# Kernel tuning notes

Hardware: AMD Instinct MI355X
Metric: run time of the kernel (lower is better)

Reference implementation:

```python
import jax, jax.numpy as jnp
import numpy as np

B, S, D, H = 2, 2048, 1024, 16
ND = D // H  # head dim = 64


def setup_inputs() -> dict:
    key = jax.random.key(0)
    ks = jax.random.split(key, 11)
    scale = 1.0 / np.sqrt(D)
    inp = {
        "q": jax.random.normal(ks[0], (B, S, D), dtype=jnp.float32),
        "k": jax.random.normal(ks[1], (B, S, D), dtype=jnp.float32),
        "v": jax.random.normal(ks[2], (B, S, D), dtype=jnp.float32),
        # causal mask, broadcast over batch and heads
        "mask": jnp.tril(jnp.ones((S, S), dtype=jnp.int32))[None, None, :, :],
        "Wq": jax.random.normal(ks[3], (D, D), dtype=jnp.float32) * scale,
        "bq": jnp.zeros((D,), dtype=jnp.float32),
        "Wk": jax.random.normal(ks[4], (D, D), dtype=jnp.float32) * scale,
        "bk": jnp.zeros((D,), dtype=jnp.float32),
        "Wv": jax.random.normal(ks[5], (D, D), dtype=jnp.float32) * scale,
        "bv": jnp.zeros((D,), dtype=jnp.float32),
        "Wo": jax.random.normal(ks[6], (D, D), dtype=jnp.float32) * scale,
        "bo": jnp.zeros((D,), dtype=jnp.float32),
    }
    return inp


def reference(q, k, v, mask, Wq, bq, Wk, bk, Wv, bv, Wo, bo):
    batch, seq_len, _ = q.shape
    # torch nn.Linear: x @ W.T + b
    qh = (q @ Wq.T + bq).reshape(batch, seq_len, H, ND).transpose(0, 2, 1, 3)
    kh = (k @ Wk.T + bk).reshape(batch, seq_len, H, ND).transpose(0, 2, 1, 3)
    vh = (v @ Wv.T + bv).reshape(batch, seq_len, H, ND).transpose(0, 2, 1, 3)
    # [B,H,S,S] scores
    score = jnp.einsum("bhqd,bhkd->bhqk", qh, kh) / jnp.sqrt(jnp.float32(ND))
    score = jnp.where(mask == 0, jnp.float32(-1e9), score)
    score = jax.nn.softmax(score, axis=-1)
    out = jnp.einsum("bhqk,bhkd->bhqd", score, vh)
    out = out.transpose(0, 2, 1, 3).reshape(batch, seq_len, D)
    return out @ Wo.T + bo
```

## Files before the change

### kernel.cpp

```cpp
#include <hip/hip_runtime.h>
#include <hip/hip_bf16.h>
#include <stdint.h>

#define S_LEN 2048
#define DMODEL 1024
#define NHEAD 16
#define HDIM 64
#define BATCH 2

typedef __bf16 bf16_t;
typedef __attribute__((ext_vector_type(8))) __bf16 bf16x8;
typedef __attribute__((ext_vector_type(4))) __bf16 bf16x4;
typedef __attribute__((ext_vector_type(4))) float f32x4;
typedef __attribute__((ext_vector_type(16))) float f32x16;
typedef __attribute__((ext_vector_type(4))) uint32_t u32x4;

#define LOG2E 1.44269504088896340736f

__device__ __forceinline__ void gload_lds16(const void* g, void* l) {
  __builtin_amdgcn_global_load_lds(
      (const __attribute__((address_space(1))) uint32_t*)g,
      (__attribute__((address_space(3))) uint32_t*)l, 16, 0, 0);
}

__global__ __launch_bounds__(256) void convert_all(
    const float* __restrict__ q, const float* __restrict__ k, const float* __restrict__ v,
    const float* __restrict__ wq, const float* __restrict__ wk, const float* __restrict__ wv,
    const float* __restrict__ wo,
    bf16_t* __restrict__ qb, bf16_t* __restrict__ kb, bf16_t* __restrict__ vb,
    bf16_t* __restrict__ wqb, bf16_t* __restrict__ wkb, bf16_t* __restrict__ wvb,
    bf16_t* __restrict__ wob)
{
  const size_t M1 = 1048576;
  size_t e = ((size_t)blockIdx.x * 256 + threadIdx.x) * 4;
  const float* src; bf16_t* dst; size_t off;
  if      (e <  4*M1) { src = q;  dst = qb;  off = e;         }
  else if (e <  8*M1) { src = k;  dst = kb;  off = e - 4*M1;  }
  else if (e < 12*M1) { src = v;  dst = vb;  off = e - 8*M1;  }
  else if (e < 13*M1) { src = wq; dst = wqb; off = e - 12*M1; }
  else if (e < 14*M1) { src = wk; dst = wkb; off = e - 13*M1; }
  else if (e < 15*M1) { src = wv; dst = wvb; off = e - 14*M1; }
  else                { src = wo; dst = wob; off = e - 15*M1; }
  float4 f = *reinterpret_cast<const float4*>(src + off);
  bf16x4 o;
  o[0] = (bf16_t)f.x; o[1] = (bf16_t)f.y; o[2] = (bf16_t)f.z; o[3] = (bf16_t)f.w;
  *reinterpret_cast<bf16x4*>(dst + off) = o;
}

__device__ __forceinline__ void gemm_body(
    const bf16_t* __restrict__ A, const bf16_t* __restrict__ W,
    const float* __restrict__ bias, bf16_t* __restrict__ outb,
    float* __restrict__ outf, int M, int N, int K, float scale, int packmode)
{
  __shared__ bf16_t As[128 * 32];
  __shared__ bf16_t Bs[128 * 32];
  int tid = threadIdx.x;
  int w = tid >> 6, lane = tid & 63;
  int lr = lane & 15, lg = lane >> 4;
  int wr = w >> 1, wc = w & 1;
  int m0 = blockIdx.x * 128, n0 = blockIdx.y * 128;

  f32x4 acc[4][4];
#pragma unroll
  for (int a = 0; a < 4; ++a)
#pragma unroll
    for (int bq = 0; bq < 4; ++bq) acc[a][bq] = (f32x4){0.f, 0.f, 0.f, 0.f};

  int col_st = (lane & 3) * 8;

  for (int kt = 0; kt < K; kt += 32) {
#pragma unroll
    for (int it = 0; it < 2; ++it) {
      int chunkbase = (w * 2 + it) * 512;
      int row = (w * 2 + it) * 16 + (lane >> 2);
      gload_lds16(A + (size_t)(m0 + row) * K + kt + col_st, &As[chunkbase]);
      gload_lds16(W + (size_t)(n0 + row) * K + kt + col_st, &Bs[chunkbase]);
    }
    __syncthreads();
    bf16x8 af[4], bfv[4];
#pragma unroll
    for (int mf = 0; mf < 4; ++mf)
      af[mf] = *reinterpret_cast<const bf16x8*>(&As[(wr * 64 + mf * 16 + lr) * 32 + lg * 8]);
#pragma unroll
    for (int nf = 0; nf < 4; ++nf)
      bfv[nf] = *reinterpret_cast<const bf16x8*>(&Bs[(wc * 64 + nf * 16 + lr) * 32 + lg * 8]);
#pragma unroll
    for (int mf = 0; mf < 4; ++mf)
#pragma unroll
      for (int nf = 0; nf < 4; ++nf)
        acc[mf][nf] = __builtin_amdgcn_mfma_f32_16x16x32_bf16(af[mf], bfv[nf], acc[mf][nf], 0, 0, 0);
    __syncthreads();
  }

#pragma unroll
  for (int mf = 0; mf < 4; ++mf) {
#pragma unroll
    for (int nf = 0; nf < 4; ++nf) {
      int col = n0 + wc * 64 + nf * 16 + lr;
      float bcol = bias[col];
#pragma unroll
      for (int i = 0; i < 4; ++i) {
        int row = m0 + wr * 64 + mf * 16 + lg * 4 + i;
        float vv = (acc[mf][nf][i] + bcol) * scale;
        if (outf) {
          outf[(size_t)row * N + col] = vv;
        } else if (packmode == 0) {
          outb[(size_t)row * N + col] = (bf16_t)vv;
        } else if (packmode == 1) {
          int hh = col >> 6, dh = col & 63;
          int ks = dh >> 4, hi2 = (dh >> 3) & 1, jj = dh & 7;
          int bb2 = row >> 11, sK = row & 2047;
          int bh = bb2 * 16 + hh;
          size_t off = ((size_t)(bh * 64 + (sK >> 5)) * 8 + ks * 2 + hi2) * 256
                     + (size_t)(sK & 31) * 8 + jj;
          outb[off] = (bf16_t)vv;
        } else {
          int hh = col >> 6, d = col & 63;
          int db = d >> 5, dlo = d & 31;
          int bb2 = row >> 11, sK = row & 2047;
          int t32 = sK >> 5, kvin = sK & 31;
          int s2 = kvin >> 4, hi2 = (kvin >> 3) & 1, jj = kvin & 7;
          int bh = bb2 * 16 + hh;
          size_t off = ((size_t)(bh * 64 + t32) * 4 + s2 * 2 + db) * 512
                     + (size_t)(hi2 * 32 + dlo) * 8 + jj;
          outb[off] = (bf16_t)vv;
        }
      }
    }
  }
}

__global__ __launch_bounds__(256) void gemm_proj(
    const bf16_t* __restrict__ qb, const bf16_t* __restrict__ kb, const bf16_t* __restrict__ vb,
    const bf16_t* __restrict__ wqb, const bf16_t* __restrict__ wkb, const bf16_t* __restrict__ wvb,
    const float* __restrict__ bq, const float* __restrict__ bk, const float* __restrict__ bv,
    bf16_t* __restrict__ Qp, bf16_t* __restrict__ Kpk, bf16_t* __restrict__ Vpk)
{
  int z = blockIdx.z;
  const bf16_t* A = (z == 0) ? qb : (z == 1) ? kb : vb;
  const bf16_t* W = (z == 0) ? wqb : (z == 1) ? wkb : wvb;
  const float* bias = (z == 0) ? bq : (z == 1) ? bk : bv;
  bf16_t* o = (z == 0) ? Qp : (z == 1) ? Kpk : Vpk;
  float scale = (z == 0) ? 0.125f * LOG2E : 1.0f;
  gemm_body(A, W, bias, o, nullptr, BATCH * S_LEN, DMODEL, DMODEL, scale, z);
}

__global__ __launch_bounds__(256) void gemm_out(
    const bf16_t* __restrict__ O, const bf16_t* __restrict__ wob,
    const float* __restrict__ bo, float* __restrict__ out)
{
  gemm_body(O, wob, bo, nullptr, out, BATCH * S_LEN, DMODEL, DMODEL, 1.0f, 0);
}

__global__ __launch_bounds__(256, 2) void attn_fwd(
    const bf16_t* __restrict__ Qp, const bf16_t* __restrict__ Kpk,
    const bf16_t* __restrict__ Vpk, bf16_t* __restrict__ O)
{
  int flat = blockIdx.x;
  int bh = flat & 31, qp = flat >> 5;
  int b = bh >> 4, h = bh & 15;
  int tid = threadIdx.x, wv = tid >> 6, lane = tid & 63;
  int ql = lane & 31, hi = lane >> 5;
  int s = wv >> 1, hf = wv & 1;

  __shared__ float Om[2][64][35];

  const bf16_t* Kbh = Kpk + (size_t)bh * 131072 + lane * 8;
  const bf16_t* Vbh = Vpk + (size_t)bh * 131072 + lane * 8;

  for (int p = 0; p < 2; ++p) {
    int qt64 = p ? (31 - qp) : qp;
    int qbase = qt64 * 64 + s * 32;
    int q_row = qbase + ql;
    int t_diag = qbase >> 5;
    int t0 = hf ? (qt64 + 1) : 0;
    int t1 = hf ? (2 * qt64 + 2) : (qt64 + 1);
    t1 = (t1 < t_diag + 1) ? t1 : (t_diag + 1);

    const bf16_t* Qb = Qp + ((size_t)b * S_LEN + q_row) * DMODEL + h * HDIM + hi * 8;
    bf16x8 qf[4];
#pragma unroll
    for (int ks = 0; ks < 4; ++ks)
      qf[ks] = *reinterpret_cast<const bf16x8*>(Qb + ks * 16);

    f32x16 oacc0 = (f32x16)(0.0f);
    f32x16 oacc1 = (f32x16)(0.0f);
    float m = -1e30f, l = 0.f;

    for (int t = t0; t < t1; ++t) {
      const bf16_t* Kt = Kbh + (size_t)t * 2048;
      const bf16_t* Vt = Vbh + (size_t)t * 2048;

      bf16x8 kf[4], vf[4];
#pragma unroll
      for (int f = 0; f < 4; ++f)
        kf[f] = *reinterpret_cast<const bf16x8*>(Kt + f * 512);
#pragma unroll
      for (int f = 0; f < 4; ++f)
        vf[f] = *reinterpret_cast<const bf16x8*>(Vt + f * 512);

      f32x16 sa = (f32x16)(0.0f);
      __builtin_amdgcn_s_setprio(1);
      sa = __builtin_amdgcn_mfma_f32_32x32x16_bf16(kf[0], qf[0], sa, 0, 0, 0);
      sa = __builtin_amdgcn_mfma_f32_32x32x16_bf16(kf[1], qf[1], sa, 0, 0, 0);
      sa = __builtin_amdgcn_mfma_f32_32x32x16_bf16(kf[2], qf[2], sa, 0, 0, 0);
      sa = __builtin_amdgcn_mfma_f32_32x32x16_bf16(kf[3], qf[3], sa, 0, 0, 0);
      __builtin_amdgcn_s_setprio(0);

      if (t == t_diag) {
#pragma unroll
        for (int r = 0; r < 16; ++r) {
          int kvl = (r & 3) + 8 * (r >> 2) + 4 * hi;
          if (kvl > ql) sa[r] = -1e30f;
        }
      }

      float lmax = sa[0];
#pragma unroll
      for (int r = 1; r < 16; ++r) lmax = fmaxf(lmax, sa[r]);
      if (__any(lmax > m + 8.f)) {
        float mx = fmaxf(lmax, __shfl_xor(lmax, 32));
        float mn = fmaxf(m, mx);
        float rsc = __builtin_amdgcn_exp2f(m - mn);
        m = mn; l *= rsc;
        oacc0 *= rsc;
        oacc1 *= rsc;
      }

      float pr[16];
      float psum = 0.f;
#pragma unroll
      for (int r = 0; r < 16; ++r) {
        pr[r] = __builtin_amdgcn_exp2f(sa[r] - m);
        psum += pr[r];
      }
      l += psum;

      uint32_t w[8];
#pragma unroll
      for (int kk = 0; kk < 8; ++kk) {
        bf16_t plo = (bf16_t)pr[2 * kk], phi = (bf16_t)pr[2 * kk + 1];
        w[kk] = (uint32_t)__builtin_bit_cast(unsigned short, plo)
              | ((uint32_t)__builtin_bit_cast(unsigned short, phi) << 16);
      }

      __builtin_amdgcn_s_setprio(1);
      {
        uint32_t u0  = hi ? w[2] : w[0], u1  = hi ? w[3] : w[1];
        uint32_t sd0 = hi ? w[0] : w[2], sd1 = hi ? w[1] : w[3];
        uint32_t x0 = __shfl_xor(sd0, 32), x1 = __shfl_xor(sd1, 32);
        u32x4 pw = { hi ? x0 : u0, hi ? x1 : u1, hi ? u0 : x0, hi ? u1 : x1 };
        bf16x8 pf = __builtin_bit_cast(bf16x8, pw);
        oacc0 = __builtin_amdgcn_mfma_f32_32x32x16_bf16(vf[0], pf, oacc0, 0, 0, 0);
        oacc1 = __builtin_amdgcn_mfma_f32_32x32x16_bf16(vf[1], pf, oacc1, 0, 0, 0);
      }
      {
        uint32_t u0  = hi ? w[6] : w[4], u1  = hi ? w[7] : w[5];
        uint32_t sd0 = hi ? w[4] : w[6], sd1 = hi ? w[5] : w[7];
        uint32_t x0 = __shfl_xor(sd0, 32), x1 = __shfl_xor(sd1, 32);
        u32x4 pw = { hi ? x0 : u0, hi ? x1 : u1, hi ? u0 : x0, hi ? u1 : x1 };
        bf16x8 pf = __builtin_bit_cast(bf16x8, pw);
        oacc0 = __builtin_amdgcn_mfma_f32_32x32x16_bf16(vf[2], pf, oacc0, 0, 0, 0);
        oacc1 = __builtin_amdgcn_mfma_f32_32x32x16_bf16(vf[3], pf, oacc1, 0, 0, 0);
      }
      __builtin_amdgcn_s_setprio(0);
    }

    if (hf) {
      Om[s][lane][0] = m;
      Om[s][lane][1] = l;
#pragma unroll
      for (int r = 0; r < 16; ++r) {
        Om[s][lane][2 + r]  = oacc0[r];
        Om[s][lane][18 + r] = oacc1[r];
      }
    }
    __syncthreads();
    if (!hf) {
      float mB = Om[s][lane][0], lB = Om[s][lane][1];
      float mAB = fmaxf(m, mB);
      float fA = __builtin_amdgcn_exp2f(m - mAB);
      float fB = __builtin_amdgcn_exp2f(mB - mAB);
      l = l * fA + lB * fB;
#pragma unroll
      for (int r = 0; r < 16; ++r) {
        oacc0[r] = oacc0[r] * fA + Om[s][lane][2 + r]  * fB;
        oacc1[r] = oacc1[r] * fA + Om[s][lane][18 + r] * fB;
      }
      l += __shfl_xor(l, 32);
      float inv = 1.0f / l;
      bf16_t* ob = O + ((size_t)b * S_LEN + q_row) * DMODEL + h * HDIM;
#pragma unroll
      for (int g = 0; g < 4; ++g) {
        bf16x4 ov0, ov1;
#pragma unroll
        for (int i = 0; i < 4; ++i) {
          ov0[i] = (bf16_t)(oacc0[4 * g + i] * inv);
          ov1[i] = (bf16_t)(oacc1[4 * g + i] * inv);
        }
        *reinterpret_cast<bf16x4*>(ob + 8 * g + 4 * hi)      = ov0;
        *reinterpret_cast<bf16x4*>(ob + 32 + 8 * g + 4 * hi) = ov1;
      }
    }
    __syncthreads();
  }
}

extern "C" void kernel_launch(void* const* d_in, const int* in_sizes, int n_in,
                              void* d_out, int out_size, void* d_ws, size_t ws_size,
                              hipStream_t stream) {
  const float* q  = (const float*)d_in[0];
  const float* k  = (const float*)d_in[1];
  const float* v  = (const float*)d_in[2];
  const float* Wq = (const float*)d_in[4];
  const float* bq = (const float*)d_in[5];
  const float* Wk = (const float*)d_in[6];
  const float* bk = (const float*)d_in[7];
  const float* Wv = (const float*)d_in[8];
  const float* bv = (const float*)d_in[9];
  const float* Wo = (const float*)d_in[10];
  const float* bo = (const float*)d_in[11];
  float* out = (float*)d_out;

  const size_t MB = 1u << 20;
  char* base = (char*)d_ws;
  bf16_t* qb  = (bf16_t*)(base + 0 * MB);
  bf16_t* kb  = (bf16_t*)(base + 8 * MB);
  bf16_t* vb  = (bf16_t*)(base + 16 * MB);
  bf16_t* wqb = (bf16_t*)(base + 24 * MB);
  bf16_t* wkb = (bf16_t*)(base + 26 * MB);
  bf16_t* wvb = (bf16_t*)(base + 28 * MB);
  bf16_t* wob = (bf16_t*)(base + 30 * MB);
  bf16_t* Qp  = (bf16_t*)(base + 32 * MB);
  bf16_t* Kpk = (bf16_t*)(base + 40 * MB);
  bf16_t* Vpk = (bf16_t*)(base + 48 * MB);
  bf16_t* Ob  = (bf16_t*)(base + 56 * MB);

  convert_all<<<16384, 256, 0, stream>>>(q, k, v, Wq, Wk, Wv, Wo,
                                         qb, kb, vb, wqb, wkb, wvb, wob);
  gemm_proj<<<dim3(32, 8, 3), 256, 0, stream>>>(qb, kb, vb, wqb, wkb, wvb,
                                                bq, bk, bv, Qp, Kpk, Vpk);
  attn_fwd<<<512, 256, 0, stream>>>(Qp, Kpk, Vpk, Ob);
  gemm_out<<<dim3(32, 8), 256, 0, stream>>>(Ob, wob, bo, out);
}
```

Before: 113.2 us.

## Rewrite QKV projection GEMM with 256x256 tiles, double-buffered swizzled LDS

The QKV projection GEMM now uses 512-thread blocks with 256x256 output tiles and K-step 64. Global-to-LDS loads are double-buffered and issued in halves between compute phases, with explicit vmcnt waits and barriers. LDS reads use an XOR swizzle to avoid bank conflicts, and the MFMA bursts run at raised priority. The goal is to hide load latency and raise data reuse per tile. The cost is a grid of only 192 blocks, which may underfill the GPU, plus 128KB of LDS per block.

```diff
diff --git a/kernel.cpp b/kernel.cpp
--- a/kernel.cpp
+++ b/kernel.cpp
@@ -47,90 +47,36 @@
   *reinterpret_cast<bf16x4*>(dst + off) = o;
 }
 
-__device__ __forceinline__ void gemm_body(
-    const bf16_t* __restrict__ A, const bf16_t* __restrict__ W,
-    const float* __restrict__ bias, bf16_t* __restrict__ outb,
-    float* __restrict__ outf, int M, int N, int K, float scale, int packmode)
+__device__ __forceinline__ void pack_store(
+    bf16_t* __restrict__ outb, float* __restrict__ outf,
+    int packmode, int row, int col, int N, float vv)
 {
-  __shared__ bf16_t As[128 * 32];
-  __shared__ bf16_t Bs[128 * 32];
-  int tid = threadIdx.x;
-  int w = tid >> 6, lane = tid & 63;
-  int lr = lane & 15, lg = lane >> 4;
-  int wr = w >> 1, wc = w & 1;
-  int m0 = blockIdx.x * 128, n0 = blockIdx.y * 128;
-
-  f32x4 acc[4][4];
-#pragma unroll
-  for (int a = 0; a < 4; ++a)
-#pragma unroll
-    for (int bq = 0; bq < 4; ++bq) acc[a][bq] = (f32x4){0.f, 0.f, 0.f, 0.f};
-
-  int col_st = (lane & 3) * 8;
-
-  for (int kt = 0; kt < K; kt += 32) {
-#pragma unroll
-    for (int it = 0; it < 2; ++it) {
-      int chunkbase = (w * 2 + it) * 512;
-      int row = (w * 2 + it) * 16 + (lane >> 2);
-      gload_lds16(A + (size_t)(m0 + row) * K + kt + col_st, &As[chunkbase]);
-      gload_lds16(W + (size_t)(n0 + row) * K + kt + col_st, &Bs[chunkbase]);
-    }
-    __syncthreads();
-    bf16x8 af[4], bfv[4];
-#pragma unroll
-    for (int mf = 0; mf < 4; ++mf)
-      af[mf] = *reinterpret_cast<const bf16x8*>(&As[(wr * 64 + mf * 16 + lr) * 32 + lg * 8]);
-#pragma unroll
-    for (int nf = 0; nf < 4; ++nf)
-      bfv[nf] = *reinterpret_cast<const bf16x8*>(&Bs[(wc * 64 + nf * 16 + lr) * 32 + lg * 8]);
-#pragma unroll
-    for (int mf = 0; mf < 4; ++mf)
-#pragma unroll
-      for (int nf = 0; nf < 4; ++nf)
-        acc[mf][nf] = __builtin_amdgcn_mfma_f32_16x16x32_bf16(af[mf], bfv[nf], acc[mf][nf], 0, 0, 0);
-    __syncthreads();
-  }
-
-#pragma unroll
-  for (int mf = 0; mf < 4; ++mf) {
-#pragma unroll
-    for (int nf = 0; nf < 4; ++nf) {
-      int col = n0 + wc * 64 + nf * 16 + lr;
-      float bcol = bias[col];
-#pragma unroll
-      for (int i = 0; i < 4; ++i) {
-        int row = m0 + wr * 64 + mf * 16 + lg * 4 + i;
-        float vv = (acc[mf][nf][i] + bcol) * scale;
-        if (outf) {
-          outf[(size_t)row * N + col] = vv;
-        } else if (packmode == 0) {
-          outb[(size_t)row * N + col] = (bf16_t)vv;
-        } else if (packmode == 1) {
-          int hh = col >> 6, dh = col & 63;
-          int ks = dh >> 4, hi2 = (dh >> 3) & 1, jj = dh & 7;
-          int bb2 = row >> 11, sK = row & 2047;
-          int bh = bb2 * 16 + hh;
-          size_t off = ((size_t)(bh * 64 + (sK >> 5)) * 8 + ks * 2 + hi2) * 256
-                     + (size_t)(sK & 31) * 8 + jj;
-          outb[off] = (bf16_t)vv;
-        } else {
-          int hh = col >> 6, d = col & 63;
-          int db = d >> 5, dlo = d & 31;
-          int bb2 = row >> 11, sK = row & 2047;
-          int t32 = sK >> 5, kvin = sK & 31;
-          int s2 = kvin >> 4, hi2 = (kvin >> 3) & 1, jj = kvin & 7;
-          int bh = bb2 * 16 + hh;
-          size_t off = ((size_t)(bh * 64 + t32) * 4 + s2 * 2 + db) * 512
-                     + (size_t)(hi2 * 32 + dlo) * 8 + jj;
-          outb[off] = (bf16_t)vv;
-        }
-      }
-    }
-  }
-}
-
-__global__ __launch_bounds__(256) void gemm_proj(
+  if (outf) {
+    outf[(size_t)row * N + col] = vv;
+  } else if (packmode == 0) {
+    outb[(size_t)row * N + col] = (bf16_t)vv;
+  } else if (packmode == 1) {
+    int hh = col >> 6, dh = col & 63;
+    int ks = dh >> 4, hi2 = (dh >> 3) & 1, jj = dh & 7;
+    int bb2 = row >> 11, sK = row & 2047;
+    int bh = bb2 * 16 + hh;
+    size_t off = ((size_t)(bh * 64 + (sK >> 5)) * 8 + ks * 2 + hi2) * 256
+               + (size_t)(sK & 31) * 8 + jj;
+    outb[off] = (bf16_t)vv;
+  } else {
+    int hh = col >> 6, d = col & 63;
+    int db = d >> 5, dlo = d & 31;
+    int bb2 = row >> 11, sK = row & 2047;
+    int t32 = sK >> 5, kvin = sK & 31;
+    int s2 = kvin >> 4, hi2 = (kvin >> 3) & 1, jj = kvin & 7;
+    int bh = bb2 * 16 + hh;
+    size_t off = ((size_t)(bh * 64 + t32) * 4 + s2 * 2 + db) * 512
+               + (size_t)(hi2 * 32 + dlo) * 8 + jj;
+    outb[off] = (bf16_t)vv;
+  }
+}
+
+__global__ __launch_bounds__(512, 2) void gemm_proj(
     const bf16_t* __restrict__ qb, const bf16_t* __restrict__ kb, const bf16_t* __restrict__ vb,
     const bf16_t* __restrict__ wqb, const bf16_t* __restrict__ wkb, const bf16_t* __restrict__ wvb,
     const float* __restrict__ bq, const float* __restrict__ bk, const float* __restrict__ bv,
@@ -140,16 +86,192 @@
   const bf16_t* A = (z == 0) ? qb : (z == 1) ? kb : vb;
   const bf16_t* W = (z == 0) ? wqb : (z == 1) ? wkb : wvb;
   const float* bias = (z == 0) ? bq : (z == 1) ? bk : bv;
-  bf16_t* o = (z == 0) ? Qp : (z == 1) ? Kpk : Vpk;
+  bf16_t* outb = (z == 0) ? Qp : (z == 1) ? Kpk : Vpk;
   float scale = (z == 0) ? 0.125f * LOG2E : 1.0f;
-  gemm_body(A, W, bias, o, nullptr, BATCH * S_LEN, DMODEL, DMODEL, scale, z);
+
+  const int K = DMODEL;
+  const int NT = K / 64;
+
+  __shared__ bf16_t LA[2][2][8192];
+  __shared__ bf16_t LB[2][2][8192];
+
+  int tid = threadIdx.x;
+  int wid = tid >> 6, lane = tid & 63;
+  int wm = wid >> 2, wn = wid & 3;
+  int lr = lane & 15, lg = lane >> 4;
+  int m0 = blockIdx.x * 256, n0 = blockIdx.y * 256;
+
+  int rsub = lane >> 3;
+  int csw = ((lane & 7) ^ (rsub & 7)) * 8;
+  const bf16_t* aRow = A + (size_t)(m0 + wid * 8 + rsub) * K + csw;
+  const bf16_t* bRow = W + (size_t)(n0 + wid * 8 + rsub) * K + csw;
+  int ldsW = wid * 512;
+
+#define STG_A(tt, h, buf)                                                      \
+  do {                                                                         \
+    gload_lds16(aRow + (size_t)(h) * 128 * 1024 + (tt) * 64,                   \
+                &LA[buf][h][ldsW]);                                            \
+    gload_lds16(aRow + (size_t)(h) * 128 * 1024 + 64 * 1024 + (tt) * 64,       \
+                &LA[buf][h][ldsW + 4096]);                                     \
+  } while (0)
+#define STG_B(tt, h, buf)                                                      \
+  do {                                                                         \
+    gload_lds16(bRow + (size_t)(h) * 128 * 1024 + (tt) * 64,                   \
+                &LB[buf][h][ldsW]);                                            \
+    gload_lds16(bRow + (size_t)(h) * 128 * 1024 + 64 * 1024 + (tt) * 64,       \
+                &LB[buf][h][ldsW + 4096]);                                     \
+  } while (0)
+
+  f32x4 acc[8][4];
+#pragma unroll
+  for (int i = 0; i < 8; ++i)
+#pragma unroll
+    for (int j = 0; j < 4; ++j) acc[i][j] = (f32x4){0.f, 0.f, 0.f, 0.f};
+
+  STG_A(0, 0, 0); STG_B(0, 0, 0);
+  STG_A(0, 1, 0); STG_B(0, 1, 0);
+
+  int lrx = lr & 7;
+
+  for (int t = 0; t < NT; ++t) {
+    int cur = t & 1;
+    bf16_t* la = &LA[cur][wm][0];
+    bf16_t* lb = &LB[cur][wn >> 1][0];
+    int bcol = (wn & 1) * 64;
+    bool more = (t + 1 < NT);
+
+#define QPHASE(MH, NH)                                                          \
+    do {                                                                        \
+      bf16x8 af[4][2], bf[2][2];                                                \
+      _Pragma("unroll")                                                         \
+      for (int mf = 0; mf < 4; ++mf) {                                          \
+        int rowA = MH * 64 + mf * 16 + lr;                                      \
+        _Pragma("unroll")                                                       \
+        for (int ks = 0; ks < 2; ++ks)                                          \
+          af[mf][ks] = *reinterpret_cast<const bf16x8*>(                        \
+              la + rowA * 64 + (((ks * 4 + lg) ^ lrx) * 8));                    \
+      }                                                                         \
+      _Pragma("unroll")                                                         \
+      for (int nf = 0; nf < 2; ++nf) {                                          \
+        int rowB = bcol + (NH * 2 + nf) * 16 + lr;                              \
+        _Pragma("unroll")                                                       \
+        for (int ks = 0; ks < 2; ++ks)                                          \
+          bf[nf][ks] = *reinterpret_cast<const bf16x8*>(                        \
+              lb + rowB * 64 + (((ks * 4 + lg) ^ lrx) * 8));                    \
+      }                                                                         \
+      asm volatile("s_waitcnt lgkmcnt(0)" ::: "memory");                        \
+      __builtin_amdgcn_sched_barrier(0);                                        \
+      __builtin_amdgcn_s_setprio(1);                                            \
+      _Pragma("unroll")                                                         \
+      for (int mf = 0; mf < 4; ++mf)                                            \
+        _Pragma("unroll")                                                       \
+        for (int nf = 0; nf < 2; ++nf) {                                        \
+          acc[MH * 4 + mf][NH * 2 + nf] = __builtin_amdgcn_mfma_f32_16x16x32_bf16( \
+              af[mf][0], bf[nf][0], acc[MH * 4 + mf][NH * 2 + nf], 0, 0, 0);    \
+          acc[MH * 4 + mf][NH * 2 + nf] = __builtin_amdgcn_mfma_f32_16x16x32_bf16( \
+              af[mf][1], bf[nf][1], acc[MH * 4 + mf][NH * 2 + nf], 0, 0, 0);    \
+        }                                                                       \
+      __builtin_amdgcn_s_setprio(0);                                            \
+    } while (0)
+
+    asm volatile("s_waitcnt vmcnt(4)" ::: "memory");
+    __builtin_amdgcn_s_barrier();
+    if (more) { STG_A(t + 1, 0, cur ^ 1); STG_B(t + 1, 0, cur ^ 1); }
+    QPHASE(0, 0);
+
+    if (more) {
+      asm volatile("s_waitcnt vmcnt(4)" ::: "memory");
+    } else {
+      asm volatile("s_waitcnt vmcnt(0)" ::: "memory");
+    }
+    __builtin_amdgcn_s_barrier();
+    if (more) { STG_A(t + 1, 1, cur ^ 1); STG_B(t + 1, 1, cur ^ 1); }
+    QPHASE(0, 1);
+
+    __builtin_amdgcn_s_barrier();
+    QPHASE(1, 0);
+
+    __builtin_amdgcn_s_barrier();
+    QPHASE(1, 1);
+#undef QPHASE
+  }
+#undef STG_A
+#undef STG_B
+
+#pragma unroll
+  for (int mf = 0; mf < 8; ++mf) {
+#pragma unroll
+    for (int nf = 0; nf < 4; ++nf) {
+      int col = n0 + wn * 64 + nf * 16 + lr;
+      float bcolv = bias[col];
+#pragma unroll
+      for (int i = 0; i < 4; ++i) {
+        int row = m0 + wm * 128 + mf * 16 + lg * 4 + i;
+        float vv = (acc[mf][nf][i] + bcolv) * scale;
+        pack_store(outb, nullptr, z, row, col, DMODEL, vv);
+      }
+    }
+  }
 }
 
 __global__ __launch_bounds__(256) void gemm_out(
     const bf16_t* __restrict__ O, const bf16_t* __restrict__ wob,
     const float* __restrict__ bo, float* __restrict__ out)
 {
-  gemm_body(O, wob, bo, nullptr, out, BATCH * S_LEN, DMODEL, DMODEL, 1.0f, 0);
+  const int K = DMODEL, N = DMODEL;
+  __shared__ bf16_t As[128 * 32];
+  __shared__ bf16_t Bs[128 * 32];
+  int tid = threadIdx.x;
+  int w = tid >> 6, lane = tid & 63;
+  int lr = lane & 15, lg = lane >> 4;
+  int wr = w >> 1, wc = w & 1;
+  int m0 = blockIdx.x * 128, n0 = blockIdx.y * 128;
+
+  f32x4 acc[4][4];
+#pragma unroll
+  for (int a = 0; a < 4; ++a)
+#pragma unroll
+    for (int bq = 0; bq < 4; ++bq) acc[a][bq] = (f32x4){0.f, 0.f, 0.f, 0.f};
+
+  int col_st = (lane & 3) * 8;
+
+  for (int kt = 0; kt < K; kt += 32) {
+#pragma unroll
+    for (int it = 0; it < 2; ++it) {
+      int chunkbase = (w * 2 + it) * 512;
+      int row = (w * 2 + it) * 16 + (lane >> 2);
+      gload_lds16(O + (size_t)(m0 + row) * K + kt + col_st, &As[chunkbase]);
+      gload_lds16(wob + (size_t)(n0 + row) * K + kt + col_st, &Bs[chunkbase]);
+    }
+    __syncthreads();
+    bf16x8 af[4], bfv[4];
+#pragma unroll
+    for (int mf = 0; mf < 4; ++mf)
+      af[mf] = *reinterpret_cast<const bf16x8*>(&As[(wr * 64 + mf * 16 + lr) * 32 + lg * 8]);
+#pragma unroll
+    for (int nf = 0; nf < 4; ++nf)
+      bfv[nf] = *reinterpret_cast<const bf16x8*>(&Bs[(wc * 64 + nf * 16 + lr) * 32 + lg * 8]);
+#pragma unroll
+    for (int mf = 0; mf < 4; ++mf)
+#pragma unroll
+      for (int nf = 0; nf < 4; ++nf)
+        acc[mf][nf] = __builtin_amdgcn_mfma_f32_16x16x32_bf16(af[mf], bfv[nf], acc[mf][nf], 0, 0, 0);
+    __syncthreads();
+  }
+
+#pragma unroll
+  for (int mf = 0; mf < 4; ++mf) {
+#pragma unroll
+    for (int nf = 0; nf < 4; ++nf) {
+      int col = n0 + wc * 64 + nf * 16 + lr;
+      float bcol = bo[col];
+#pragma unroll
+      for (int i = 0; i < 4; ++i) {
+        int row = m0 + wr * 64 + mf * 16 + lg * 4 + i;
+        out[(size_t)row * N + col] = acc[mf][nf][i] + bcol;
+      }
+    }
+  }
 }
 
 __global__ __launch_bounds__(256, 2) void attn_fwd(
@@ -338,7 +460,7 @@
 
   convert_all<<<16384, 256, 0, stream>>>(q, k, v, Wq, Wk, Wv, Wo,
                                          qb, kb, vb, wqb, wkb, wvb, wob);
-  gemm_proj<<<dim3(32, 8, 3), 256, 0, stream>>>(qb, kb, vb, wqb, wkb, wvb,
+  gemm_proj<<<dim3(16, 4, 3), 512, 0, stream>>>(qb, kb, vb, wqb, wkb, wvb,
                                                 bq, bk, bv, Qp, Kpk, Vpk);
   attn_fwd<<<512, 256, 0, stream>>>(Qp, Kpk, Vpk, Ob);
   gemm_out<<<dim3(32, 8), 256, 0, stream>>>(Ob, wob, bo, out);
```

After: 129.1 us. +14.0%, slower.

## Double GEMM K-tile to 64 with XOR-swizzled LDS layout

Applied to the files above, without the earlier changes.

The shared GEMM body now stages 64-wide K slices of A and W per iteration instead of 32, which halves the number of barrier pairs per output tile. The LDS rows are stored with an XOR swizzle on the 16-byte column chunk, and the fragment reads use the matching swizzle, so MFMA operand loads avoid LDS bank conflicts. Each thread issues four async global-to-LDS loads per matrix per iteration and holds twice the fragment registers. LDS use doubles to 32 KB per block, which may lower occupancy. The epilogue store logic is moved into a helper function with the same behavior.

```diff
diff --git a/kernel.cpp b/kernel.cpp
--- a/kernel.cpp
+++ b/kernel.cpp
@@ -47,13 +47,42 @@
   *reinterpret_cast<bf16x4*>(dst + off) = o;
 }
 
+__device__ __forceinline__ void pack_store(
+    bf16_t* __restrict__ outb, float* __restrict__ outf,
+    int packmode, int row, int col, int N, float vv)
+{
+  if (outf) {
+    outf[(size_t)row * N + col] = vv;
+  } else if (packmode == 0) {
+    outb[(size_t)row * N + col] = (bf16_t)vv;
+  } else if (packmode == 1) {
+    int hh = col >> 6, dh = col & 63;
+    int ks = dh >> 4, hi2 = (dh >> 3) & 1, jj = dh & 7;
+    int bb2 = row >> 11, sK = row & 2047;
+    int bh = bb2 * 16 + hh;
+    size_t off = ((size_t)(bh * 64 + (sK >> 5)) * 8 + ks * 2 + hi2) * 256
+               + (size_t)(sK & 31) * 8 + jj;
+    outb[off] = (bf16_t)vv;
+  } else {
+    int hh = col >> 6, d = col & 63;
+    int db = d >> 5, dlo = d & 31;
+    int bb2 = row >> 11, sK = row & 2047;
+    int t32 = sK >> 5, kvin = sK & 31;
+    int s2 = kvin >> 4, hi2 = (kvin >> 3) & 1, jj = kvin & 7;
+    int bh = bb2 * 16 + hh;
+    size_t off = ((size_t)(bh * 64 + t32) * 4 + s2 * 2 + db) * 512
+               + (size_t)(hi2 * 32 + dlo) * 8 + jj;
+    outb[off] = (bf16_t)vv;
+  }
+}
+
 __device__ __forceinline__ void gemm_body(
     const bf16_t* __restrict__ A, const bf16_t* __restrict__ W,
     const float* __restrict__ bias, bf16_t* __restrict__ outb,
     float* __restrict__ outf, int M, int N, int K, float scale, int packmode)
 {
-  __shared__ bf16_t As[128 * 32];
-  __shared__ bf16_t Bs[128 * 32];
+  __shared__ bf16_t As[128 * 64];
+  __shared__ bf16_t Bs[128 * 64];
   int tid = threadIdx.x;
   int w = tid >> 6, lane = tid & 63;
   int lr = lane & 15, lg = lane >> 4;
@@ -66,29 +95,41 @@
 #pragma unroll
     for (int bq = 0; bq < 4; ++bq) acc[a][bq] = (f32x4){0.f, 0.f, 0.f, 0.f};
 
-  int col_st = (lane & 3) * 8;
-
-  for (int kt = 0; kt < K; kt += 32) {
-#pragma unroll
-    for (int it = 0; it < 2; ++it) {
-      int chunkbase = (w * 2 + it) * 512;
-      int row = (w * 2 + it) * 16 + (lane >> 2);
-      gload_lds16(A + (size_t)(m0 + row) * K + kt + col_st, &As[chunkbase]);
-      gload_lds16(W + (size_t)(n0 + row) * K + kt + col_st, &Bs[chunkbase]);
+  int rsub = lane >> 3;
+  int csw = ((lane & 7) ^ rsub) * 8;
+  int lrx = lr & 7;
+
+  for (int kt = 0; kt < K; kt += 64) {
+#pragma unroll
+    for (int it = 0; it < 4; ++it) {
+      int rbase = w * 32 + it * 8;
+      int row = rbase + rsub;
+      gload_lds16(A + (size_t)(m0 + row) * K + kt + csw, &As[rbase * 64]);
+      gload_lds16(W + (size_t)(n0 + row) * K + kt + csw, &Bs[rbase * 64]);
     }
     __syncthreads();
-    bf16x8 af[4], bfv[4];
+    bf16x8 af[4][2], bfv[4][2];
+#pragma unroll
+    for (int mf = 0; mf < 4; ++mf) {
+      int rowA = (wr * 64 + mf * 16 + lr) * 64;
+#pragma unroll
+      for (int ks = 0; ks < 2; ++ks)
+        af[mf][ks] = *reinterpret_cast<const bf16x8*>(&As[rowA + (((ks * 4 + lg) ^ lrx) * 8)]);
+    }
+#pragma unroll
+    for (int nf = 0; nf < 4; ++nf) {
+      int rowB = (wc * 64 + nf * 16 + lr) * 64;
+#pragma unroll
+      for (int ks = 0; ks < 2; ++ks)
+        bfv[nf][ks] = *reinterpret_cast<const bf16x8*>(&Bs[rowB + (((ks * 4 + lg) ^ lrx) * 8)]);
+    }
 #pragma unroll
     for (int mf = 0; mf < 4; ++mf)
-      af[mf] = *reinterpret_cast<const bf16x8*>(&As[(wr * 64 + mf * 16 + lr) * 32 + lg * 8]);
-#pragma unroll
-    for (int nf = 0; nf < 4; ++nf)
-      bfv[nf] = *reinterpret_cast<const bf16x8*>(&Bs[(wc * 64 + nf * 16 + lr) * 32 + lg * 8]);
-#pragma unroll
-    for (int mf = 0; mf < 4; ++mf)
-#pragma unroll
-      for (int nf = 0; nf < 4; ++nf)
-        acc[mf][nf] = __builtin_amdgcn_mfma_f32_16x16x32_bf16(af[mf], bfv[nf], acc[mf][nf], 0, 0, 0);
+#pragma unroll
+      for (int nf = 0; nf < 4; ++nf) {
+        acc[mf][nf] = __builtin_amdgcn_mfma_f32_16x16x32_bf16(af[mf][0], bfv[nf][0], acc[mf][nf], 0, 0, 0);
+        acc[mf][nf] = __builtin_amdgcn_mfma_f32_16x16x32_bf16(af[mf][1], bfv[nf][1], acc[mf][nf], 0, 0, 0);
+      }
     __syncthreads();
   }
 
@@ -102,29 +143,7 @@
       for (int i = 0; i < 4; ++i) {
         int row = m0 + wr * 64 + mf * 16 + lg * 4 + i;
         float vv = (acc[mf][nf][i] + bcol) * scale;
-        if (outf) {
-          outf[(size_t)row * N + col] = vv;
-        } else if (packmode == 0) {
-          outb[(size_t)row * N + col] = (bf16_t)vv;
-        } else if (packmode == 1) {
-          int hh = col >> 6, dh = col & 63;
-          int ks = dh >> 4, hi2 = (dh >> 3) & 1, jj = dh & 7;
-          int bb2 = row >> 11, sK = row & 2047;
-          int bh = bb2 * 16 + hh;
-          size_t off = ((size_t)(bh * 64 + (sK >> 5)) * 8 + ks * 2 + hi2) * 256
-                     + (size_t)(sK & 31) * 8 + jj;
-          outb[off] = (bf16_t)vv;
-        } else {
-          int hh = col >> 6, d = col & 63;
-          int db = d >> 5, dlo = d & 31;
-          int bb2 = row >> 11, sK = row & 2047;
-          int t32 = sK >> 5, kvin = sK & 31;
-          int s2 = kvin >> 4, hi2 = (kvin >> 3) & 1, jj = kvin & 7;
-          int bh = bb2 * 16 + hh;
-          size_t off = ((size_t)(bh * 64 + t32) * 4 + s2 * 2 + db) * 512
-                     + (size_t)(hi2 * 32 + dlo) * 8 + jj;
-          outb[off] = (bf16_t)vv;
-        }
+        pack_store(outb, outf, packmode, row, col, N, vv);
       }
     }
   }
```

After: 123.3 us. +8.9%, slower.
